# Performance work log

Measured on AMD Instinct MI355X. Metric: run time of the kernel, lower is better.

## Reference

```python
import jax, jax.numpy as jnp
import numpy as np

N_HEAD, D_HEAD, D_MODEL, MAX_LEN = 16, 64, 1024, 64
T, B = 1024, 4
SCALE = 1.0 / D_HEAD ** 0.5


def setup_inputs() -> dict:
    key = jax.random.key(0)
    k1, k2, k3, k4 = jax.random.split(key, 4)
    s = 0.02
    w = jax.random.normal(k1, (T, B, D_MODEL), jnp.float32)
    Wqkv = jax.random.normal(k2, (3 * N_HEAD * D_HEAD, D_MODEL), jnp.float32) * s
    pos_emb = jax.random.normal(k3, (2 * MAX_LEN + 1, D_HEAD), jnp.float32) * s
    Wo = jax.random.normal(k4, (D_MODEL, N_HEAD * D_HEAD), jnp.float32) * s
    i = jnp.arange(T)
    # causal mask, 3D path of the original: [qlen, klen, bsz], True = masked
    attn_mask = jnp.broadcast_to((i[None, :] > i[:, None])[:, :, None], (T, T, B))
    return {"w": w, "attn_mask": attn_mask, "Wqkv": Wqkv, "pos_emb": pos_emb, "Wo": Wo}


def reference(w, attn_mask, Wqkv, pos_emb, Wo):
    qlen, bsz, _ = w.shape
    klen = qlen
    # qkv projection (no bias), chunk into q, k, v
    heads = jnp.einsum('tbd,ed->tbe', w, Wqkv)            # [T, B, 3*H*Dh]
    q, k, v = jnp.split(heads, 3, axis=-1)
    q = q.reshape(qlen, bsz, N_HEAD, D_HEAD).transpose(1, 2, 0, 3) * SCALE  # [B,H,T,Dh]
    k = k.reshape(klen, bsz, N_HEAD, D_HEAD).transpose(1, 2, 0, 3)
    v = v.reshape(klen, bsz, N_HEAD, D_HEAD).transpose(1, 2, 0, 3)
    # learnable relative position embeddings r[q_pos, k_pos, Dh]
    i = jnp.arange(klen)
    rel = jnp.clip(i[None, :] - i[:, None], -MAX_LEN, MAX_LEN) + MAX_LEN   # [T, T]
    r = pos_emb[rel]                                                       # [T, T, Dh]
    # content score + relative-position score (q already scaled)
    qk = jnp.einsum('bhqd,bhkd->bhqk', q, k)
    qr = jnp.einsum('bhqd,qkd->bhqk', q, r)
    score = qk + qr                                                        # [B,H,T,T]
    m = attn_mask.transpose(2, 0, 1)[:, None]                              # [B,1,T,T]
    score = jnp.where(m, -jnp.inf, score)
    attn = jax.nn.softmax(score, axis=-1)                                  # coverage
    # content context + position context
    ctx = jnp.einsum('bhqk,bhkd->bhqd', attn, v) + jnp.einsum('bhqk,qkd->bhqd', attn, r)
    attn_vec = ctx.transpose(0, 2, 1, 3).reshape(bsz, qlen, N_HEAD * D_HEAD)
    out = jnp.einsum('bte,de->btd', attn_vec, Wo)                          # [B,T,D]
    return jnp.swapaxes(out, 0, 1)                                         # [T,B,D]
```

## Files before the change

### kernel.cpp

```cpp
#include <hip/hip_runtime.h>
#include <hip/hip_bf16.h>
#include <math.h>

#define N_HEAD 16
#define D_HEAD 64
#define T_SEQ 1024
#define BATCH 4
#define QSCALE 0.180336879f

typedef float f32x4 __attribute__((ext_vector_type(4)));
typedef short bf16x8 __attribute__((ext_vector_type(8)));
typedef short bf16x4v __attribute__((ext_vector_type(4)));

#define AS1(p) ((const __attribute__((address_space(1))) void*)(p))
#define AS3(p) ((__attribute__((address_space(3))) void*)(p))

__device__ inline bf16x8 ld8(const __hip_bfloat16* p) {
    bf16x4v lo = *(const bf16x4v*)p;
    bf16x4v hi = *(const bf16x4v*)(p + 4);
    return __builtin_shufflevector(lo, hi, 0, 1, 2, 3, 4, 5, 6, 7);
}

__global__ __launch_bounds__(256) void cast_all(
    const float* __restrict__ s0, __hip_bfloat16* __restrict__ d0, int n0,
    const float* __restrict__ s1, __hip_bfloat16* __restrict__ d1, int n1) {
    int i = (blockIdx.x * 256 + threadIdx.x) * 8;
    const float* src;
    __hip_bfloat16* dst;
    if (i < n0) { src = s0 + i; dst = d0 + i; }
    else if ((i -= n0) < n1) { src = s1 + i; dst = d1 + i; }
    else return;
    float4 a = *(const float4*)src;
    float4 b = *(const float4*)(src + 4);
    __hip_bfloat16 t[8];
    t[0] = __float2bfloat16(a.x); t[1] = __float2bfloat16(a.y);
    t[2] = __float2bfloat16(a.z); t[3] = __float2bfloat16(a.w);
    t[4] = __float2bfloat16(b.x); t[5] = __float2bfloat16(b.y);
    t[6] = __float2bfloat16(b.z); t[7] = __float2bfloat16(b.w);
    *(uint4*)dst = *(const uint4*)t;
}

__global__ __launch_bounds__(256) void qkv_gemm_mfma(
    const __hip_bfloat16* __restrict__ A,
    const __hip_bfloat16* __restrict__ B,
    const float* __restrict__ P,
    __hip_bfloat16* __restrict__ Qb, __hip_bfloat16* __restrict__ Kb,
    __hip_bfloat16* __restrict__ Vtb) {
    constexpr int Kd = 1024;
    __shared__ __hip_bfloat16 As[128 * 32];
    __shared__ __hip_bfloat16 Bs[128 * 32];
    const int tid = threadIdx.x;
    const int w = tid >> 6, lane = tid & 63;
    const int lanelo = lane & 15, quad = lane >> 4;
    const int wm = (w >> 1) * 64, wn = (w & 1) * 64;
    const int m0 = blockIdx.y * 128, n0 = blockIdx.x * 128;

    const __hip_bfloat16* Ag = A + (size_t)(m0 + w * 16 + (lane >> 2)) * Kd + (lane & 3) * 8;
    const __hip_bfloat16* Bg = B + (size_t)(n0 + w * 16 + (lane >> 2)) * Kd + (lane & 3) * 8;
    __hip_bfloat16* AsW0 = As + w * 16 * 32;
    __hip_bfloat16* AsW1 = As + (64 + w * 16) * 32;
    __hip_bfloat16* BsW0 = Bs + w * 16 * 32;
    __hip_bfloat16* BsW1 = Bs + (64 + w * 16) * 32;

    f32x4 acc[4][4];
#pragma unroll
    for (int i = 0; i < 4; i++)
#pragma unroll
        for (int j = 0; j < 4; j++) acc[i][j] = (f32x4){0.f, 0.f, 0.f, 0.f};

    for (int k0 = 0; k0 < Kd; k0 += 32) {
        __syncthreads();
        __builtin_amdgcn_global_load_lds(AS1(Ag + k0), AS3(AsW0), 16, 0, 0);
        __builtin_amdgcn_global_load_lds(AS1(Ag + 64 * Kd + k0), AS3(AsW1), 16, 0, 0);
        __builtin_amdgcn_global_load_lds(AS1(Bg + k0), AS3(BsW0), 16, 0, 0);
        __builtin_amdgcn_global_load_lds(AS1(Bg + 64 * Kd + k0), AS3(BsW1), 16, 0, 0);
        __syncthreads();
        bf16x8 af[4], bfr[4];
#pragma unroll
        for (int i = 0; i < 4; i++)
            af[i] = *(const bf16x8*)(As + (wm + i * 16 + lanelo) * 32 + quad * 8);
#pragma unroll
        for (int j = 0; j < 4; j++)
            bfr[j] = *(const bf16x8*)(Bs + (wn + j * 16 + lanelo) * 32 + quad * 8);
#pragma unroll
        for (int i = 0; i < 4; i++)
#pragma unroll
            for (int j = 0; j < 4; j++)
                acc[i][j] = __builtin_amdgcn_mfma_f32_16x16x32_bf16(af[i], bfr[j], acc[i][j], 0, 0, 0);
    }

    const int part = n0 >> 10;
    float p0v[4] = {0.f, 0.f, 0.f, 0.f};
    if (part == 2) {
#pragma unroll
        for (int j = 0; j < 4; j++) p0v[j] = P[j * 16 + lanelo];
    }
#pragma unroll
    for (int i = 0; i < 4; i++)
#pragma unroll
        for (int j = 0; j < 4; j++)
#pragma unroll
            for (int reg = 0; reg < 4; reg++) {
                const int row = m0 + wm + i * 16 + quad * 4 + reg;
                const int col = n0 + wn + j * 16 + lanelo;
                const int t = row >> 2, b = row & 3;
                const int e = col & 1023, h = e >> 6, d = e & 63;
                const float v = acc[i][j][reg];
                if (part == 0)
                    Qb[((size_t)(b * 16 + h) * 1024 + t) * 64 + d] = __float2bfloat16(v * QSCALE);
                else if (part == 1)
                    Kb[((size_t)(b * 16 + h) * 1024 + t) * 64 + d] = __float2bfloat16(v);
                else
                    Vtb[((size_t)(b * 16 + h) * 64 + d) * 1024 + t] = __float2bfloat16(v + p0v[j]);
            }
}

__global__ __launch_bounds__(256) void out_gemm_mfma(
    const __hip_bfloat16* __restrict__ A,
    const __hip_bfloat16* __restrict__ B,
    float* __restrict__ out) {
    constexpr int Kd = 1024;
    __shared__ __hip_bfloat16 As[128 * 64];
    __shared__ __hip_bfloat16 Bs[64 * 64];
    const int tid = threadIdx.x;
    const int w = tid >> 6, lane = tid & 63;
    const int lanelo = lane & 15, quad = lane >> 4;
    const int wm = (w >> 1) * 64, wn = (w & 1) * 32;
    const int m0 = blockIdx.y * 128, n0 = blockIdx.x * 64;

    const int sr = lane >> 3;
    const int sc = ((lane & 7) ^ sr) * 8;
    const __hip_bfloat16* Ag = A + (size_t)(m0 + w * 32 + sr) * Kd + sc;
    const __hip_bfloat16* Bg = B + (size_t)(n0 + w * 16 + sr) * Kd + sc;
    __hip_bfloat16* AsW = As + w * 2048;
    __hip_bfloat16* BsW = Bs + w * 1024;

    f32x4 acc[4][2];
#pragma unroll
    for (int i = 0; i < 4; i++)
#pragma unroll
        for (int j = 0; j < 2; j++) acc[i][j] = (f32x4){0.f, 0.f, 0.f, 0.f};

    const int cswz = lanelo & 7;

    for (int k0 = 0; k0 < Kd; k0 += 64) {
        __syncthreads();
#pragma unroll
        for (int i = 0; i < 4; i++)
            __builtin_amdgcn_global_load_lds(AS1(Ag + k0 + i * 8 * Kd), AS3(AsW + i * 512), 16, 0, 0);
#pragma unroll
        for (int i = 0; i < 2; i++)
            __builtin_amdgcn_global_load_lds(AS1(Bg + k0 + i * 8 * Kd), AS3(BsW + i * 512), 16, 0, 0);
        __syncthreads();
#pragma unroll
        for (int h = 0; h < 2; h++) {
            const int c16 = (((h * 4 + quad) ^ cswz)) * 8;
            bf16x8 af[4], bfr[2];
#pragma unroll
            for (int i = 0; i < 4; i++)
                af[i] = *(const bf16x8*)(As + (size_t)(wm + i * 16 + lanelo) * 64 + c16);
#pragma unroll
            for (int j = 0; j < 2; j++)
                bfr[j] = *(const bf16x8*)(Bs + (size_t)(wn + j * 16 + lanelo) * 64 + c16);
#pragma unroll
            for (int i = 0; i < 4; i++)
#pragma unroll
                for (int j = 0; j < 2; j++)
                    acc[i][j] = __builtin_amdgcn_mfma_f32_16x16x32_bf16(af[i], bfr[j], acc[i][j], 0, 0, 0);
        }
    }

#pragma unroll
    for (int i = 0; i < 4; i++)
#pragma unroll
        for (int j = 0; j < 2; j++)
#pragma unroll
            for (int reg = 0; reg < 4; reg++) {
                const int row = m0 + wm + i * 16 + quad * 4 + reg;
                const int col = n0 + wn + j * 16 + lanelo;
                const int b = row >> 10, t = row & 1023;
                out[(size_t)(t * 4 + b) * 1024 + col] = acc[i][j][reg];
            }
}

__global__ __launch_bounds__(256) void flash_attn(
    const __hip_bfloat16* __restrict__ Qb,
    const __hip_bfloat16* __restrict__ Kb,
    const __hip_bfloat16* __restrict__ Vtb,
    const float* __restrict__ P,
    const float* __restrict__ Wo,
    __hip_bfloat16* __restrict__ Wob,
    __hip_bfloat16* __restrict__ av) {
    __shared__ __hip_bfloat16 Ks[64][72];
    __shared__ __hip_bfloat16 Vs[64][72];
    __shared__ __hip_bfloat16 Pl[4][16][68];
    __shared__ __hip_bfloat16 Pband[4][2][16][68];
    __shared__ __hip_bfloat16 QPl[4][2][16][66];

    const int px = blockIdx.y;
    const int TB = 15 - px, TS = px;
    const int bh = blockIdx.x;
    const int b = bh >> 4, h = bh & 15;
    const int tid = threadIdx.x;

    {
        const int gid = (bh * 8 + px) * 256 + tid;
        const float4 a = *(const float4*)(Wo + (size_t)gid * 8);
        const float4 c = *(const float4*)(Wo + (size_t)gid * 8 + 4);
        __hip_bfloat16 t[8];
        t[0] = __float2bfloat16(a.x); t[1] = __float2bfloat16(a.y);
        t[2] = __float2bfloat16(a.z); t[3] = __float2bfloat16(a.w);
        t[4] = __float2bfloat16(c.x); t[5] = __float2bfloat16(c.y);
        t[6] = __float2bfloat16(c.z); t[7] = __float2bfloat16(c.w);
        *(uint4*)(Wob + (size_t)gid * 8) = *(const uint4*)t;
    }

    const int w = tid >> 6, lane = tid & 63;
    const int lanelo = lane & 15, quad = lane >> 4;
    const size_t qkbase = (size_t)bh * 1024 * 64;
    const size_t vbase  = (size_t)bh * 64 * 1024;

    const int sr = tid >> 2;
    const int sc = (tid & 3) << 4;
    const __hip_bfloat16* kgb = Kb + qkbase + (size_t)sr * 64 + sc;
    const __hip_bfloat16* vgb = Vtb + vbase + (size_t)sr * 1024 + sc;

    {
        short* pb = (short*)&Pband[w][0][0][0];
        for (int i = lane; i < 2 * 16 * 68; i += 64) pb[i] = 0;
    }

    bf16x8 aqb0, aqb1, aqs0, aqs1;
    {
        const __hip_bfloat16* qrb = Qb + qkbase + (size_t)(TB * 64 + w * 16 + lanelo) * 64;
        aqb0 = *(const bf16x8*)(qrb + quad * 8);
        aqb1 = *(const bf16x8*)(qrb + 32 + quad * 8);
        const __hip_bfloat16* qrs = Qb + qkbase + (size_t)(TS * 64 + w * 16 + lanelo) * 64;
        aqs0 = *(const bf16x8*)(qrs + quad * 8);
        aqs1 = *(const bf16x8*)(qrs + 32 + quad * 8);
    }

#pragma unroll
    for (int jj = 0; jj < 5; jj++) {
        const float* prow = P + (size_t)(jj * 16 + lanelo) * 64 + quad * 8;
        float4 pa = *(const float4*)prow;
        float4 pb = *(const float4*)(prow + 4);
        float4 pc = *(const float4*)(prow + 32);
        float4 pd = *(const float4*)(prow + 36);
        __hip_bfloat16 t0[8], t1[8];
        t0[0] = __float2bfloat16(pa.x); t0[1] = __float2bfloat16(pa.y);
        t0[2] = __float2bfloat16(pa.z); t0[3] = __float2bfloat16(pa.w);
        t0[4] = __float2bfloat16(pb.x); t0[5] = __float2bfloat16(pb.y);
        t0[6] = __float2bfloat16(pb.z); t0[7] = __float2bfloat16(pb.w);
        t1[0] = __float2bfloat16(pc.x); t1[1] = __float2bfloat16(pc.y);
        t1[2] = __float2bfloat16(pc.z); t1[3] = __float2bfloat16(pc.w);
        t1[4] = __float2bfloat16(pd.x); t1[5] = __float2bfloat16(pd.y);
        t1[6] = __float2bfloat16(pd.z); t1[7] = __float2bfloat16(pd.w);
        f32x4 accB = (f32x4){0.f, 0.f, 0.f, 0.f};
        accB = __builtin_amdgcn_mfma_f32_16x16x32_bf16(aqb0, *(const bf16x8*)t0, accB, 0, 0, 0);
        accB = __builtin_amdgcn_mfma_f32_16x16x32_bf16(aqb1, *(const bf16x8*)t1, accB, 0, 0, 0);
        f32x4 accS = (f32x4){0.f, 0.f, 0.f, 0.f};
        accS = __builtin_amdgcn_mfma_f32_16x16x32_bf16(aqs0, *(const bf16x8*)t0, accS, 0, 0, 0);
        accS = __builtin_amdgcn_mfma_f32_16x16x32_bf16(aqs1, *(const bf16x8*)t1, accS, 0, 0, 0);
#pragma unroll
        for (int reg = 0; reg < 4; reg++) {
            QPl[w][0][quad * 4 + reg][jj * 16 + lanelo] = __float2bfloat16(accB[reg]);
            QPl[w][1][quad * 4 + reg][jj * 16 + lanelo] = __float2bfloat16(accS[reg]);
        }
    }
    float qp0b[4], qp0s[4];
#pragma unroll
    for (int reg = 0; reg < 4; reg++) {
        qp0b[reg] = (float)QPl[w][0][quad * 4 + reg][0];
        qp0s[reg] = (float)QPl[w][1][quad * 4 + reg][0];
    }

    f32x4 o_accB[4], o_lB, o_accS[4], o_lS;
#pragma unroll
    for (int dt = 0; dt < 4; dt++) {
        o_accB[dt] = (f32x4){0.f, 0.f, 0.f, 0.f};
        o_accS[dt] = (f32x4){0.f, 0.f, 0.f, 0.f};
    }
    o_lB = (f32x4){0.f, 0.f, 0.f, 0.f};
    o_lS = (f32x4){0.f, 0.f, 0.f, 0.f};
    const short one_bf = 0x3F80;
    const bf16x8 vones = {one_bf, one_bf, one_bf, one_bf, one_bf, one_bf, one_bf, one_bf};

    auto do_qtile = [&](int tq, int Tq, const bf16x8& a0, const bf16x8& a1,
                        const float* qp0, f32x4* o_acc, f32x4& o_l, int kt) {
        f32x4 s_acc[4];
        __builtin_amdgcn_s_setprio(1);
#pragma unroll
        for (int ct = 0; ct < 4; ct++) {
            bf16x8 b0 = *(const bf16x8*)&Ks[ct * 16 + lanelo][quad * 8];
            bf16x8 b1 = *(const bf16x8*)&Ks[ct * 16 + lanelo][32 + quad * 8];
            f32x4 acc = (f32x4){0.f, 0.f, 0.f, 0.f};
            acc = __builtin_amdgcn_mfma_f32_16x16x32_bf16(a0, b0, acc, 0, 0, 0);
            acc = __builtin_amdgcn_mfma_f32_16x16x32_bf16(a1, b1, acc, 0, 0, 0);
            s_acc[ct] = acc;
        }
        __builtin_amdgcn_s_setprio(0);
        const int q0 = Tq * 64 + w * 16;
        const int obase = q0 - kt * 64;
        if (kt < Tq - 1) {
#pragma unroll
            for (int ct = 0; ct < 4; ct++)
#pragma unroll
                for (int reg = 0; reg < 4; reg++) {
                    const float p = __builtin_exp2f(s_acc[ct][reg] + qp0[reg]);
                    Pl[w][quad * 4 + reg][ct * 16 + lanelo] = __float2bfloat16(p);
                }
        } else {
#pragma unroll
            for (int ct = 0; ct < 4; ct++)
#pragma unroll
                for (int reg = 0; reg < 4; reg++) {
                    const int rloc = quad * 4 + reg;
                    const int kl = ct * 16 + lanelo;
                    const int o = obase + rloc - kl;
                    const int idx = (o >= 64 || o < 0) ? 0 : (64 - o);
                    const float add = (float)QPl[w][tq][rloc][idx];
                    const float p = (o < 0) ? 0.f : __builtin_exp2f(s_acc[ct][reg] + add);
                    const __hip_bfloat16 pbv = __float2bfloat16(p);
                    Pl[w][rloc][kl] = pbv;
                    if (o >= 0 && o <= 63) Pband[w][tq][rloc][63 - o] = pbv;
                }
        }
        __builtin_amdgcn_s_setprio(1);
#pragma unroll
        for (int c = 0; c < 2; c++) {
            bf16x8 ap = ld8(&Pl[w][lanelo][c * 32 + quad * 8]);
#pragma unroll
            for (int dt = 0; dt < 4; dt++) {
                bf16x8 bv = *(const bf16x8*)&Vs[dt * 16 + lanelo][c * 32 + quad * 8];
                o_acc[dt] = __builtin_amdgcn_mfma_f32_16x16x32_bf16(ap, bv, o_acc[dt], 0, 0, 0);
            }
            o_l = __builtin_amdgcn_mfma_f32_16x16x32_bf16(ap, vones, o_l, 0, 0, 0);
        }
        __builtin_amdgcn_s_setprio(0);
    };

    uint4 rk0, rk1, rv0, rv1;
    rk0 = *(const uint4*)(kgb);
    rk1 = *(const uint4*)(kgb + 8);
    rv0 = *(const uint4*)(vgb);
    rv1 = *(const uint4*)(vgb + 8);

    for (int kt = 0; kt <= TB; kt++) {
        __syncthreads();
        *(uint4*)&Ks[sr][sc]     = rk0;
        *(uint4*)&Ks[sr][sc + 8] = rk1;
        *(uint4*)&Vs[sr][sc]     = rv0;
        *(uint4*)&Vs[sr][sc + 8] = rv1;
        if (kt < TB) {
            const __hip_bfloat16* kg = kgb + (size_t)(kt + 1) * 4096;
            const __hip_bfloat16* vg = vgb + (size_t)(kt + 1) * 64;
            rk0 = *(const uint4*)(kg);
            rk1 = *(const uint4*)(kg + 8);
            rv0 = *(const uint4*)(vg);
            rv1 = *(const uint4*)(vg + 8);
        }
        __syncthreads();

        do_qtile(0, TB, aqb0, aqb1, qp0b, o_accB, o_lB, kt);
        if (kt <= TS) do_qtile(1, TS, aqs0, aqs1, qp0s, o_accS, o_lS, kt);
    }

#pragma unroll
    for (int tq = 0; tq < 2; tq++) {
        f32x4* o_acc = tq == 0 ? o_accB : o_accS;
        f32x4& o_l   = tq == 0 ? o_lB : o_lS;
        const int q0 = (tq == 0 ? TB : TS) * 64 + w * 16;
#pragma unroll
        for (int c = 0; c < 2; c++) {
            bf16x8 ab = ld8(&Pband[w][tq][lanelo][c * 32 + quad * 8]);
#pragma unroll
            for (int dt = 0; dt < 4; dt++) {
                const int d = dt * 16 + lanelo;
                const float p0 = P[d];
                __hip_bfloat16 tb[8];
#pragma unroll
                for (int jj = 0; jj < 8; jj++) {
                    const int kk = c * 32 + quad * 8 + jj;
                    tb[jj] = __float2bfloat16(P[(kk + 1) * 64 + d] - p0);
                }
                o_acc[dt] = __builtin_amdgcn_mfma_f32_16x16x32_bf16(ab, *(const bf16x8*)tb, o_acc[dt], 0, 0, 0);
            }
        }
        float rinv[4];
#pragma unroll
        for (int reg = 0; reg < 4; reg++) rinv[reg] = 1.0f / o_l[reg];
#pragma unroll
        for (int dt = 0; dt < 4; dt++) {
            const int cdim = dt * 16 + lanelo;
#pragma unroll
            for (int reg = 0; reg < 4; reg++) {
                const int q = q0 + quad * 4 + reg;
                av[((size_t)(b * 1024 + q)) * 1024 + h * 64 + cdim] =
                    __float2bfloat16(o_acc[dt][reg] * rinv[reg]);
            }
        }
    }
}

extern "C" void kernel_launch(void* const* d_in, const int* in_sizes, int n_in,
                              void* d_out, int out_size, void* d_ws, size_t ws_size,
                              hipStream_t stream) {
    const float* w       = (const float*)d_in[0];
    const float* Wqkv    = (const float*)d_in[2];
    const float* pos_emb = (const float*)d_in[3];
    const float* Wo      = (const float*)d_in[4];
    float* out = (float*)d_out;

    const size_t SZ = (size_t)BATCH * N_HEAD * T_SEQ * D_HEAD;
    __hip_bfloat16* wb     = (__hip_bfloat16*)d_ws;
    __hip_bfloat16* Wqkvb  = wb + SZ;
    __hip_bfloat16* Wob    = Wqkvb + 3 * 1024 * 1024;
    __hip_bfloat16* Qb     = Wob + 1024 * 1024;
    __hip_bfloat16* Kb     = Qb + SZ;
    __hip_bfloat16* Vtb    = Kb + SZ;
    __hip_bfloat16* AVb    = Vtb + SZ;

    const int n_w = 4096 * 1024, n_wqkv = 3072 * 1024;
    const int n_tot = n_w + n_wqkv;
    cast_all<<<n_tot / 2048, 256, 0, stream>>>(w, wb, n_w, Wqkv, Wqkvb, n_wqkv);

    qkv_gemm_mfma<<<dim3(3072 / 128, 4096 / 128), 256, 0, stream>>>(wb, Wqkvb, pos_emb, Qb, Kb, Vtb);
    flash_attn<<<dim3(64, 8), 256, 0, stream>>>(Qb, Kb, Vtb, pos_emb, Wo, Wob, AVb);
    out_gemm_mfma<<<dim3(1024 / 64, 4096 / 128), 256, 0, stream>>>(AVb, Wob, out);
}
```

Before: 185.8 us.

## Read K and V tiles directly from global memory instead of LDS staging

Removes the shared-memory K/V tiles, the register-prefetch double buffering and both per-iteration __syncthreads, so each wave loads MFMA operands for K and transposed V straight from global memory. This drops LDS traffic and block-wide barriers. In exchange, all four waves and both query tiles reload the same K/V data from global memory or cache, and nothing prefetches ahead any more, so load latency sits directly in front of the MFMAs.

```diff
diff --git a/kernel.cpp b/kernel.cpp
--- a/kernel.cpp
+++ b/kernel.cpp
@@ -191,8 +191,6 @@
     const float* __restrict__ Wo,
     __hip_bfloat16* __restrict__ Wob,
     __hip_bfloat16* __restrict__ av) {
-    __shared__ __hip_bfloat16 Ks[64][72];
-    __shared__ __hip_bfloat16 Vs[64][72];
     __shared__ __hip_bfloat16 Pl[4][16][68];
     __shared__ __hip_bfloat16 Pband[4][2][16][68];
     __shared__ __hip_bfloat16 QPl[4][2][16][66];
@@ -219,11 +217,6 @@
     const int lanelo = lane & 15, quad = lane >> 4;
     const size_t qkbase = (size_t)bh * 1024 * 64;
     const size_t vbase  = (size_t)bh * 64 * 1024;
-
-    const int sr = tid >> 2;
-    const int sc = (tid & 3) << 4;
-    const __hip_bfloat16* kgb = Kb + qkbase + (size_t)sr * 64 + sc;
-    const __hip_bfloat16* vgb = Vtb + vbase + (size_t)sr * 1024 + sc;
 
     {
         short* pb = (short*)&Pband[w][0][0][0];
@@ -288,12 +281,15 @@
 
     auto do_qtile = [&](int tq, int Tq, const bf16x8& a0, const bf16x8& a1,
                         const float* qp0, f32x4* o_acc, f32x4& o_l, int kt) {
+        const __hip_bfloat16* ktile = Kb + qkbase + (size_t)kt * 64 * 64;
+        const __hip_bfloat16* vtile = Vtb + vbase + (size_t)kt * 64;
         f32x4 s_acc[4];
         __builtin_amdgcn_s_setprio(1);
 #pragma unroll
         for (int ct = 0; ct < 4; ct++) {
-            bf16x8 b0 = *(const bf16x8*)&Ks[ct * 16 + lanelo][quad * 8];
-            bf16x8 b1 = *(const bf16x8*)&Ks[ct * 16 + lanelo][32 + quad * 8];
+            const __hip_bfloat16* krow = ktile + (size_t)(ct * 16 + lanelo) * 64;
+            bf16x8 b0 = *(const bf16x8*)(krow + quad * 8);
+            bf16x8 b1 = *(const bf16x8*)(krow + 32 + quad * 8);
             f32x4 acc = (f32x4){0.f, 0.f, 0.f, 0.f};
             acc = __builtin_amdgcn_mfma_f32_16x16x32_bf16(a0, b0, acc, 0, 0, 0);
             acc = __builtin_amdgcn_mfma_f32_16x16x32_bf16(a1, b1, acc, 0, 0, 0);
@@ -332,7 +328,7 @@
             bf16x8 ap = ld8(&Pl[w][lanelo][c * 32 + quad * 8]);
 #pragma unroll
             for (int dt = 0; dt < 4; dt++) {
-                bf16x8 bv = *(const bf16x8*)&Vs[dt * 16 + lanelo][c * 32 + quad * 8];
+                bf16x8 bv = *(const bf16x8*)(vtile + (size_t)(dt * 16 + lanelo) * 1024 + c * 32 + quad * 8);
                 o_acc[dt] = __builtin_amdgcn_mfma_f32_16x16x32_bf16(ap, bv, o_acc[dt], 0, 0, 0);
             }
             o_l = __builtin_amdgcn_mfma_f32_16x16x32_bf16(ap, vones, o_l, 0, 0, 0);
@@ -340,28 +336,7 @@
         __builtin_amdgcn_s_setprio(0);
     };
 
-    uint4 rk0, rk1, rv0, rv1;
-    rk0 = *(const uint4*)(kgb);
-    rk1 = *(const uint4*)(kgb + 8);
-    rv0 = *(const uint4*)(vgb);
-    rv1 = *(const uint4*)(vgb + 8);
-
     for (int kt = 0; kt <= TB; kt++) {
-        __syncthreads();
-        *(uint4*)&Ks[sr][sc]     = rk0;
-        *(uint4*)&Ks[sr][sc + 8] = rk1;
-        *(uint4*)&Vs[sr][sc]     = rv0;
-        *(uint4*)&Vs[sr][sc + 8] = rv1;
-        if (kt < TB) {
-            const __hip_bfloat16* kg = kgb + (size_t)(kt + 1) * 4096;
-            const __hip_bfloat16* vg = vgb + (size_t)(kt + 1) * 64;
-            rk0 = *(const uint4*)(kg);
-            rk1 = *(const uint4*)(kg + 8);
-            rv0 = *(const uint4*)(vg);
-            rv1 = *(const uint4*)(vg + 8);
-        }
-        __syncthreads();
-
         do_qtile(0, TB, aqb0, aqb1, qp0b, o_accB, o_lB, kt);
         if (kt <= TS) do_qtile(1, TS, aqs0, aqs1, qp0s, o_accS, o_lS, kt);
     }
```

New measurement: 214.3 us. 15.3% more time.

## Split paired causal query tiles into one tile per attention block

Applied to the files above, without the earlier changes.

Each attention block now handles a single 64-row query tile instead of pairing a long tile with a short one for causal load balancing. The grid doubles to 64x16 blocks, and the Wo cast work is redistributed so each thread converts four floats. This gives more, smaller blocks and halves per-block register and shared-memory state, which may raise occupancy. The cost is uneven block lengths, with the longest-running blocks setting the tail, and K/V tiles reloaded once per query tile rather than shared by two.

```diff
diff --git a/kernel.cpp b/kernel.cpp
--- a/kernel.cpp
+++ b/kernel.cpp
@@ -194,25 +194,21 @@
     __shared__ __hip_bfloat16 Ks[64][72];
     __shared__ __hip_bfloat16 Vs[64][72];
     __shared__ __hip_bfloat16 Pl[4][16][68];
-    __shared__ __hip_bfloat16 Pband[4][2][16][68];
-    __shared__ __hip_bfloat16 QPl[4][2][16][66];
-
-    const int px = blockIdx.y;
-    const int TB = 15 - px, TS = px;
+    __shared__ __hip_bfloat16 Pband[4][16][68];
+    __shared__ __hip_bfloat16 QPl[4][16][66];
+
     const int bh = blockIdx.x;
+    const int Tq = 15 - blockIdx.y;
     const int b = bh >> 4, h = bh & 15;
     const int tid = threadIdx.x;
 
     {
-        const int gid = (bh * 8 + px) * 256 + tid;
-        const float4 a = *(const float4*)(Wo + (size_t)gid * 8);
-        const float4 c = *(const float4*)(Wo + (size_t)gid * 8 + 4);
-        __hip_bfloat16 t[8];
+        const int gid = (blockIdx.y * 64 + bh) * 256 + tid;
+        const float4 a = *(const float4*)(Wo + (size_t)gid * 4);
+        __hip_bfloat16 t[4];
         t[0] = __float2bfloat16(a.x); t[1] = __float2bfloat16(a.y);
         t[2] = __float2bfloat16(a.z); t[3] = __float2bfloat16(a.w);
-        t[4] = __float2bfloat16(c.x); t[5] = __float2bfloat16(c.y);
-        t[6] = __float2bfloat16(c.z); t[7] = __float2bfloat16(c.w);
-        *(uint4*)(Wob + (size_t)gid * 8) = *(const uint4*)t;
+        *(uint2*)(Wob + (size_t)gid * 4) = *(const uint2*)t;
     }
 
     const int w = tid >> 6, lane = tid & 63;
@@ -226,18 +222,15 @@
     const __hip_bfloat16* vgb = Vtb + vbase + (size_t)sr * 1024 + sc;
 
     {
-        short* pb = (short*)&Pband[w][0][0][0];
-        for (int i = lane; i < 2 * 16 * 68; i += 64) pb[i] = 0;
-    }
-
-    bf16x8 aqb0, aqb1, aqs0, aqs1;
+        short* pb = (short*)&Pband[w][0][0];
+        for (int i = lane; i < 16 * 68; i += 64) pb[i] = 0;
+    }
+
+    bf16x8 aq0, aq1;
     {
-        const __hip_bfloat16* qrb = Qb + qkbase + (size_t)(TB * 64 + w * 16 + lanelo) * 64;
-        aqb0 = *(const bf16x8*)(qrb + quad * 8);
-        aqb1 = *(const bf16x8*)(qrb + 32 + quad * 8);
-        const __hip_bfloat16* qrs = Qb + qkbase + (size_t)(TS * 64 + w * 16 + lanelo) * 64;
-        aqs0 = *(const bf16x8*)(qrs + quad * 8);
-        aqs1 = *(const bf16x8*)(qrs + 32 + quad * 8);
+        const __hip_bfloat16* qr = Qb + qkbase + (size_t)(Tq * 64 + w * 16 + lanelo) * 64;
+        aq0 = *(const bf16x8*)(qr + quad * 8);
+        aq1 = *(const bf16x8*)(qr + 32 + quad * 8);
     }
 
 #pragma unroll
@@ -256,89 +249,23 @@
         t1[2] = __float2bfloat16(pc.z); t1[3] = __float2bfloat16(pc.w);
         t1[4] = __float2bfloat16(pd.x); t1[5] = __float2bfloat16(pd.y);
         t1[6] = __float2bfloat16(pd.z); t1[7] = __float2bfloat16(pd.w);
-        f32x4 accB = (f32x4){0.f, 0.f, 0.f, 0.f};
-        accB = __builtin_amdgcn_mfma_f32_16x16x32_bf16(aqb0, *(const bf16x8*)t0, accB, 0, 0, 0);
-        accB = __builtin_amdgcn_mfma_f32_16x16x32_bf16(aqb1, *(const bf16x8*)t1, accB, 0, 0, 0);
-        f32x4 accS = (f32x4){0.f, 0.f, 0.f, 0.f};
-        accS = __builtin_amdgcn_mfma_f32_16x16x32_bf16(aqs0, *(const bf16x8*)t0, accS, 0, 0, 0);
-        accS = __builtin_amdgcn_mfma_f32_16x16x32_bf16(aqs1, *(const bf16x8*)t1, accS, 0, 0, 0);
-#pragma unroll
-        for (int reg = 0; reg < 4; reg++) {
-            QPl[w][0][quad * 4 + reg][jj * 16 + lanelo] = __float2bfloat16(accB[reg]);
-            QPl[w][1][quad * 4 + reg][jj * 16 + lanelo] = __float2bfloat16(accS[reg]);
-        }
-    }
-    float qp0b[4], qp0s[4];
-#pragma unroll
-    for (int reg = 0; reg < 4; reg++) {
-        qp0b[reg] = (float)QPl[w][0][quad * 4 + reg][0];
-        qp0s[reg] = (float)QPl[w][1][quad * 4 + reg][0];
-    }
-
-    f32x4 o_accB[4], o_lB, o_accS[4], o_lS;
-#pragma unroll
-    for (int dt = 0; dt < 4; dt++) {
-        o_accB[dt] = (f32x4){0.f, 0.f, 0.f, 0.f};
-        o_accS[dt] = (f32x4){0.f, 0.f, 0.f, 0.f};
-    }
-    o_lB = (f32x4){0.f, 0.f, 0.f, 0.f};
-    o_lS = (f32x4){0.f, 0.f, 0.f, 0.f};
+        f32x4 accQ = (f32x4){0.f, 0.f, 0.f, 0.f};
+        accQ = __builtin_amdgcn_mfma_f32_16x16x32_bf16(aq0, *(const bf16x8*)t0, accQ, 0, 0, 0);
+        accQ = __builtin_amdgcn_mfma_f32_16x16x32_bf16(aq1, *(const bf16x8*)t1, accQ, 0, 0, 0);
+#pragma unroll
+        for (int reg = 0; reg < 4; reg++)
+            QPl[w][quad * 4 + reg][jj * 16 + lanelo] = __float2bfloat16(accQ[reg]);
+    }
+    float qp0[4];
+#pragma unroll
+    for (int reg = 0; reg < 4; reg++) qp0[reg] = (float)QPl[w][quad * 4 + reg][0];
+
+    f32x4 o_acc[4], o_l;
+#pragma unroll
+    for (int dt = 0; dt < 4; dt++) o_acc[dt] = (f32x4){0.f, 0.f, 0.f, 0.f};
+    o_l = (f32x4){0.f, 0.f, 0.f, 0.f};
     const short one_bf = 0x3F80;
     const bf16x8 vones = {one_bf, one_bf, one_bf, one_bf, one_bf, one_bf, one_bf, one_bf};
-
-    auto do_qtile = [&](int tq, int Tq, const bf16x8& a0, const bf16x8& a1,
-                        const float* qp0, f32x4* o_acc, f32x4& o_l, int kt) {
-        f32x4 s_acc[4];
-        __builtin_amdgcn_s_setprio(1);
-#pragma unroll
-        for (int ct = 0; ct < 4; ct++) {
-            bf16x8 b0 = *(const bf16x8*)&Ks[ct * 16 + lanelo][quad * 8];
-            bf16x8 b1 = *(const bf16x8*)&Ks[ct * 16 + lanelo][32 + quad * 8];
-            f32x4 acc = (f32x4){0.f, 0.f, 0.f, 0.f};
-            acc = __builtin_amdgcn_mfma_f32_16x16x32_bf16(a0, b0, acc, 0, 0, 0);
-            acc = __builtin_amdgcn_mfma_f32_16x16x32_bf16(a1, b1, acc, 0, 0, 0);
-            s_acc[ct] = acc;
-        }
-        __builtin_amdgcn_s_setprio(0);
-        const int q0 = Tq * 64 + w * 16;
-        const int obase = q0 - kt * 64;
-        if (kt < Tq - 1) {
-#pragma unroll
-            for (int ct = 0; ct < 4; ct++)
-#pragma unroll
-                for (int reg = 0; reg < 4; reg++) {
-                    const float p = __builtin_exp2f(s_acc[ct][reg] + qp0[reg]);
-                    Pl[w][quad * 4 + reg][ct * 16 + lanelo] = __float2bfloat16(p);
-                }
-        } else {
-#pragma unroll
-            for (int ct = 0; ct < 4; ct++)
-#pragma unroll
-                for (int reg = 0; reg < 4; reg++) {
-                    const int rloc = quad * 4 + reg;
-                    const int kl = ct * 16 + lanelo;
-                    const int o = obase + rloc - kl;
-                    const int idx = (o >= 64 || o < 0) ? 0 : (64 - o);
-                    const float add = (float)QPl[w][tq][rloc][idx];
-                    const float p = (o < 0) ? 0.f : __builtin_exp2f(s_acc[ct][reg] + add);
-                    const __hip_bfloat16 pbv = __float2bfloat16(p);
-                    Pl[w][rloc][kl] = pbv;
-                    if (o >= 0 && o <= 63) Pband[w][tq][rloc][63 - o] = pbv;
-                }
-        }
-        __builtin_amdgcn_s_setprio(1);
-#pragma unroll
-        for (int c = 0; c < 2; c++) {
-            bf16x8 ap = ld8(&Pl[w][lanelo][c * 32 + quad * 8]);
-#pragma unroll
-            for (int dt = 0; dt < 4; dt++) {
-                bf16x8 bv = *(const bf16x8*)&Vs[dt * 16 + lanelo][c * 32 + quad * 8];
-                o_acc[dt] = __builtin_amdgcn_mfma_f32_16x16x32_bf16(ap, bv, o_acc[dt], 0, 0, 0);
-            }
-            o_l = __builtin_amdgcn_mfma_f32_16x16x32_bf16(ap, vones, o_l, 0, 0, 0);
-        }
-        __builtin_amdgcn_s_setprio(0);
-    };
 
     uint4 rk0, rk1, rv0, rv1;
     rk0 = *(const uint4*)(kgb);
@@ -346,13 +273,13 @@
     rv0 = *(const uint4*)(vgb);
     rv1 = *(const uint4*)(vgb + 8);
 
-    for (int kt = 0; kt <= TB; kt++) {
+    for (int kt = 0; kt <= Tq; kt++) {
         __syncthreads();
         *(uint4*)&Ks[sr][sc]     = rk0;
         *(uint4*)&Ks[sr][sc + 8] = rk1;
         *(uint4*)&Vs[sr][sc]     = rv0;
         *(uint4*)&Vs[sr][sc + 8] = rv1;
-        if (kt < TB) {
+        if (kt < Tq) {
             const __hip_bfloat16* kg = kgb + (size_t)(kt + 1) * 4096;
             const __hip_bfloat16* vg = vgb + (size_t)(kt + 1) * 64;
             rk0 = *(const uint4*)(kg);
@@ -362,18 +289,63 @@
         }
         __syncthreads();
 
-        do_qtile(0, TB, aqb0, aqb1, qp0b, o_accB, o_lB, kt);
-        if (kt <= TS) do_qtile(1, TS, aqs0, aqs1, qp0s, o_accS, o_lS, kt);
-    }
-
-#pragma unroll
-    for (int tq = 0; tq < 2; tq++) {
-        f32x4* o_acc = tq == 0 ? o_accB : o_accS;
-        f32x4& o_l   = tq == 0 ? o_lB : o_lS;
-        const int q0 = (tq == 0 ? TB : TS) * 64 + w * 16;
+        f32x4 s_acc[4];
+        __builtin_amdgcn_s_setprio(1);
+#pragma unroll
+        for (int ct = 0; ct < 4; ct++) {
+            bf16x8 b0 = *(const bf16x8*)&Ks[ct * 16 + lanelo][quad * 8];
+            bf16x8 b1 = *(const bf16x8*)&Ks[ct * 16 + lanelo][32 + quad * 8];
+            f32x4 acc = (f32x4){0.f, 0.f, 0.f, 0.f};
+            acc = __builtin_amdgcn_mfma_f32_16x16x32_bf16(aq0, b0, acc, 0, 0, 0);
+            acc = __builtin_amdgcn_mfma_f32_16x16x32_bf16(aq1, b1, acc, 0, 0, 0);
+            s_acc[ct] = acc;
+        }
+        __builtin_amdgcn_s_setprio(0);
+        const int q0 = Tq * 64 + w * 16;
+        const int obase = q0 - kt * 64;
+        if (kt < Tq - 1) {
+#pragma unroll
+            for (int ct = 0; ct < 4; ct++)
+#pragma unroll
+                for (int reg = 0; reg < 4; reg++) {
+                    const float p = __builtin_exp2f(s_acc[ct][reg] + qp0[reg]);
+                    Pl[w][quad * 4 + reg][ct * 16 + lanelo] = __float2bfloat16(p);
+                }
+        } else {
+#pragma unroll
+            for (int ct = 0; ct < 4; ct++)
+#pragma unroll
+                for (int reg = 0; reg < 4; reg++) {
+                    const int rloc = quad * 4 + reg;
+                    const int kl = ct * 16 + lanelo;
+                    const int o = obase + rloc - kl;
+                    const int idx = (o >= 64 || o < 0) ? 0 : (64 - o);
+                    const float add = (float)QPl[w][rloc][idx];
+                    const float p = (o < 0) ? 0.f : __builtin_exp2f(s_acc[ct][reg] + add);
+                    const __hip_bfloat16 pbv = __float2bfloat16(p);
+                    Pl[w][rloc][kl] = pbv;
+                    if (o >= 0 && o <= 63) Pband[w][rloc][63 - o] = pbv;
+                }
+        }
+        __builtin_amdgcn_s_setprio(1);
 #pragma unroll
         for (int c = 0; c < 2; c++) {
-            bf16x8 ab = ld8(&Pband[w][tq][lanelo][c * 32 + quad * 8]);
+            bf16x8 ap = ld8(&Pl[w][lanelo][c * 32 + quad * 8]);
+#pragma unroll
+            for (int dt = 0; dt < 4; dt++) {
+                bf16x8 bv = *(const bf16x8*)&Vs[dt * 16 + lanelo][c * 32 + quad * 8];
+                o_acc[dt] = __builtin_amdgcn_mfma_f32_16x16x32_bf16(ap, bv, o_acc[dt], 0, 0, 0);
+            }
+            o_l = __builtin_amdgcn_mfma_f32_16x16x32_bf16(ap, vones, o_l, 0, 0, 0);
+        }
+        __builtin_amdgcn_s_setprio(0);
+    }
+
+    {
+        const int q0 = Tq * 64 + w * 16;
+#pragma unroll
+        for (int c = 0; c < 2; c++) {
+            bf16x8 ab = ld8(&Pband[w][lanelo][c * 32 + quad * 8]);
 #pragma unroll
             for (int dt = 0; dt < 4; dt++) {
                 const int d = dt * 16 + lanelo;
@@ -426,6 +398,6 @@
     cast_all<<<n_tot / 2048, 256, 0, stream>>>(w, wb, n_w, Wqkv, Wqkvb, n_wqkv);
 
     qkv_gemm_mfma<<<dim3(3072 / 128, 4096 / 128), 256, 0, stream>>>(wb, Wqkvb, pos_emb, Qb, Kb, Vtb);
-    flash_attn<<<dim3(64, 8), 256, 0, stream>>>(Qb, Kb, Vtb, pos_emb, Wo, Wob, AVb);
+    flash_attn<<<dim3(64, 16), 256, 0, stream>>>(Qb, Kb, Vtb, pos_emb, Wo, Wob, AVb);
     out_gemm_mfma<<<dim3(1024 / 64, 4096 / 128), 256, 0, stream>>>(AVb, Wob, out);
 }
```

Measured after the change: 192.3 us. 3.5% more time.
